# Kernel optimization log

Measured on AMD Instinct MI355X. Metric: run time of the kernel, lower is better.

Reference implementation:

```python
import jax, jax.numpy as jnp
import numpy as np

D = 1024

def setup_inputs() -> dict:
    key = jax.random.key(0)
    ks = jax.random.split(key, 9)
    s = 1.0 / np.sqrt(D)
    x = jax.random.normal(ks[0], (4096, 8, D), dtype=jnp.float32)
    Wq = jax.random.uniform(ks[1], (D, D), jnp.float32, -s, s)
    bq = jax.random.uniform(ks[2], (D,), jnp.float32, -s, s)
    Wk = jax.random.uniform(ks[3], (D, D), jnp.float32, -s, s)
    bk = jax.random.uniform(ks[4], (D,), jnp.float32, -s, s)
    Wv = jax.random.uniform(ks[5], (D, D), jnp.float32, -s, s)
    bv = jax.random.uniform(ks[6], (D,), jnp.float32, -s, s)
    Wo = jax.random.uniform(ks[7], (D, D), jnp.float32, -s, s)
    bo = jax.random.uniform(ks[8], (D,), jnp.float32, -s, s)
    return {"x": x, "Wq": Wq, "bq": bq, "Wk": Wk, "bk": bk,
            "Wv": Wv, "bv": bv, "Wo": Wo, "bo": bo}

def reference(x, Wq, bq, Wk, bk, Wv, bv, Wo, bo):
    # x: (S, B, D) seq-first, matching torch module
    Q = jax.nn.elu(x @ Wq.T + bq) + 1.0  # (S,B,D)
    K = jax.nn.elu(x @ Wk.T + bk) + 1.0  # (S,B,D)
    V = x @ Wv.T + bv                    # (S,B,D)
    # KV = K^T V per batch: (B, D, D)
    KV = jnp.einsum('sbd,sbe->bde', K, V)
    # out = Q @ KV per batch, back to (S,B,D)
    out = jnp.einsum('sbd,bde->sbe', Q, KV)
    return out @ Wo.T + bo
```

## Files before the change

### kernel.cpp

```cpp
#include <hip/hip_runtime.h>


typedef __bf16 bf16;
typedef __attribute__((ext_vector_type(8))) __bf16 bf16x8;
typedef __attribute__((ext_vector_type(4))) __bf16 bf16x4;
typedef __attribute__((ext_vector_type(4))) float f32x4;

static constexpr int S = 4096;
static constexpr int B = 8;
static constexpr int D = 1024;
static constexpr int SB = S * B;
static constexpr long long NELEM = (long long)SB * D;

__device__ __forceinline__ void load_lds16(const bf16* g, void* l)
{
    __builtin_amdgcn_global_load_lds(
        (const __attribute__((address_space(1))) void*)g,
        (__attribute__((address_space(3))) void*)l, 16, 0, 0);
}

__global__ void cvt_f32_to_bf16(const float* __restrict__ in, bf16* __restrict__ out, int n)
{
    int i = (blockIdx.x * blockDim.x + threadIdx.x) * 4;
    int stride = gridDim.x * blockDim.x * 4;
    for (; i < n; i += stride) {
        float4 v = *(const float4*)(in + i);
        bf16x4 o;
        o[0] = (bf16)v.x; o[1] = (bf16)v.y; o[2] = (bf16)v.z; o[3] = (bf16)v.w;
        *(bf16x4*)(out + i) = o;
    }
}

__global__ __launch_bounds__(256) void cvt_transpose_1024(
    const float* __restrict__ in, bf16* __restrict__ out)
{
    __shared__ bf16 tile[64][72];
    const int e0 = blockIdx.y * 64;
    const int d0 = blockIdx.x * 64;
    const int t  = threadIdx.x;
    const int rl = t >> 3;
    const int c8 = (t & 7) * 8;
    #pragma unroll
    for (int p = 0; p < 2; ++p) {
        int r = rl + p * 32;
        float4 v0 = *(const float4*)(in + (long long)(e0 + r) * D + d0 + c8);
        float4 v1 = *(const float4*)(in + (long long)(e0 + r) * D + d0 + c8 + 4);
        tile[c8+0][r] = (bf16)v0.x; tile[c8+1][r] = (bf16)v0.y;
        tile[c8+2][r] = (bf16)v0.z; tile[c8+3][r] = (bf16)v0.w;
        tile[c8+4][r] = (bf16)v1.x; tile[c8+5][r] = (bf16)v1.y;
        tile[c8+6][r] = (bf16)v1.z; tile[c8+7][r] = (bf16)v1.w;
    }
    __syncthreads();
    #pragma unroll
    for (int p = 0; p < 2; ++p) {
        int dr = rl + p * 32;
        *(bf16x8*)(out + (long long)(d0 + dr) * D + e0 + c8) = *(bf16x8*)(&tile[dr][c8]);
    }
}

__global__ __launch_bounds__(256) void bvo_kernel(
    const float* __restrict__ Wo, const float* __restrict__ bv, float* __restrict__ bvo)
{
    const int row = blockIdx.x;
    const int t = threadIdx.x;
    float4 w = *(const float4*)(Wo + (long long)row * D + t * 4);
    float4 b = *(const float4*)(bv + t * 4);
    float s = w.x*b.x + w.y*b.y + w.z*b.z + w.w*b.w;
    __shared__ float red[256];
    red[t] = s; __syncthreads();
    for (int off = 128; off > 0; off >>= 1) {
        if (t < off) red[t] += red[t + off];
        __syncthreads();
    }
    if (t == 0) bvo[row] = red[0];
}

__global__ __launch_bounds__(256) void kv_add(const bf16* __restrict__ p, bf16* __restrict__ o)
{
    const long long DD = (long long)D * D;
    const int b = blockIdx.y;
    const long long i = ((long long)blockIdx.x * 256 + threadIdx.x) * 8;
    bf16x8 u = *(const bf16x8*)(p + (2 * b) * DD + i);
    bf16x8 v = *(const bf16x8*)(p + (2 * b + 1) * DD + i);
    bf16x8 r;
    #pragma unroll
    for (int j = 0; j < 8; ++j) r[j] = (bf16)((float)u[j] + (float)v[j]);
    *(bf16x8*)(o + b * DD + i) = r;
}

template<int BM, int BN, int WM, int WN, int EPI, int OUTF32, int BIASROW>
__global__ __launch_bounds__(WM * WN * 64, 2) void gemm_bt(
    const bf16* __restrict__ A, const bf16* __restrict__ Bm,
    const float* __restrict__ bias, void* __restrict__ Cout,
    int lda, int ldb, int ldc, int K,
    long long aBatch, long long bBatch, long long cBatch)
{
    constexpr int THREADS = WM * WN * 64;
    constexpr int WROWS = BM / WM, WCOLS = BN / WN;
    constexpr int MI = WROWS / 16, NI = WCOLS / 16;
    constexpr int ABYTES = BM * 64;
    constexpr int BBYTES = BN * 64;
    constexpr int BUF = ABYTES + BBYTES;

    __shared__ unsigned char smem[4 * BUF];

    const int tid  = threadIdx.x;
    const int lane = tid & 63;
    const int wave = tid >> 6;
    const int wr   = wave / WN;
    const int wc   = wave % WN;
    const int bz   = blockIdx.z;

    const int nx  = gridDim.x;
    const int bid = blockIdx.y * nx + blockIdx.x;
    const int cpx = (nx * gridDim.y) >> 3;
    const int swz = (bid & 7) * cpx + (bid >> 3);
    const long long m0 = (long long)(swz / nx) * BM;
    const long long n0 = (long long)(swz % nx) * BN;

    const bf16* Ab = A  + bz * aBatch + m0 * lda;
    const bf16* Bb = Bm + bz * bBatch + n0 * ldb;

    f32x4 acc[MI][NI] = {};
    const int NT = K >> 5;

    auto stage = [&](int t) {
        unsigned char* dst = smem + (t & 3) * BUF;
        const long long kk = (long long)t << 5;
        #pragma unroll
        for (int j = 0; j < 2; ++j) {
            const int g  = wave * 64 + lane + j * THREADS;
            const int gs = g ^ ((g >> 3) & 3);
            const int row = gs >> 2, col = (gs & 3) * 8;
            load_lds16(Ab + (long long)row * lda + kk + col,
                       dst + (wave * 64 + j * THREADS) * 16);
        }
        #pragma unroll
        for (int j = 0; j < 2; ++j) {
            const int g  = wave * 64 + lane + j * THREADS;
            const int gs = g ^ ((g >> 3) & 3);
            const int row = gs >> 2, col = (gs & 3) * 8;
            load_lds16(Bb + (long long)row * ldb + kk + col,
                       dst + ABYTES + (wave * 64 + j * THREADS) * 16);
        }
    };

    stage(0); stage(1); stage(2);

    const int ko2 = (lane >> 4) * 16;
    const int la15 = lane & 15;

    for (int t = 0; t < NT; ++t) {
        if (t + 2 < NT)      asm volatile("s_waitcnt vmcnt(8)" ::: "memory");
        else if (t + 1 < NT) asm volatile("s_waitcnt vmcnt(4)" ::: "memory");
        else                 asm volatile("s_waitcnt vmcnt(0)" ::: "memory");
        __builtin_amdgcn_s_barrier();
        asm volatile("" ::: "memory");

        if (t + 3 < NT) stage(t + 3);

        const unsigned char* buf = smem + (t & 3) * BUF;
        bf16x8 a[MI], b[NI];
        #pragma unroll
        for (int mi = 0; mi < MI; ++mi) {
            int ad = (wr * WROWS + mi * 16 + la15) * 64 + ko2;
            ad ^= ((ad >> 7) & 3) << 4;
            a[mi] = *(const bf16x8*)(buf + ad);
        }
        #pragma unroll
        for (int ni = 0; ni < NI; ++ni) {
            int ad = (wc * WCOLS + ni * 16 + la15) * 64 + ko2;
            ad ^= ((ad >> 7) & 3) << 4;
            b[ni] = *(const bf16x8*)(buf + ABYTES + ad);
        }

        __builtin_amdgcn_s_setprio(1);
        #pragma unroll
        for (int mi = 0; mi < MI; ++mi)
            #pragma unroll
            for (int ni = 0; ni < NI; ++ni)
                acc[mi][ni] = __builtin_amdgcn_mfma_f32_16x16x32_bf16(
                    a[mi], b[ni], acc[mi][ni], 0, 0, 0);
        __builtin_amdgcn_s_setprio(0);
    }

    const int crow = (lane >> 4) * 4;
    const int ccol = lane & 15;
    #pragma unroll
    for (int ni = 0; ni < NI; ++ni) {
        const long long c = n0 + wc * WCOLS + ni * 16 + ccol;
        float bcol = 0.0f;
        if (!BIASROW && bias) bcol = bias[c];
        #pragma unroll
        for (int mi = 0; mi < MI; ++mi) {
            const long long r0 = m0 + wr * WROWS + mi * 16 + crow;
            #pragma unroll
            for (int j = 0; j < 4; ++j) {
                float v = acc[mi][ni][j];
                v += BIASROW ? bias[r0 + j] : bcol;
                if (EPI == 1) v = (v > 0.0f) ? (v + 1.0f) : __expf(v);
                const long long idx = bz * cBatch + (r0 + j) * ldc + c;
                if (OUTF32) ((float*)Cout)[idx] = v;
                else        ((bf16*)Cout)[idx]  = (bf16)v;
            }
        }
    }
}

template<int EPI, int OUTF32, int BIASROW, int SPLITK>
__global__ __launch_bounds__(512, 1) void gemm8p(
    const bf16* __restrict__ A, const bf16* __restrict__ Bm,
    const float* __restrict__ bias, void* __restrict__ Cout,
    int lda, int ldb, int ldc, int K,
    long long aBatch, long long bBatch, long long cBatch)
{
    __shared__ unsigned char smem[131072];

    const int tid  = threadIdx.x;
    const int lane = tid & 63;
    const int wave = tid >> 6;
    const int wr   = wave >> 2;
    const int wc   = wave & 3;
    const int bz    = blockIdx.z;
    const int batch = bz / SPLITK;
    const int kseg  = bz % SPLITK;

    const int nx  = gridDim.x;
    const int bid = blockIdx.y * nx + blockIdx.x;
    const int cpx = (nx * gridDim.y) >> 3;
    const int swzb = (bid & 7) * cpx + (bid >> 3);
    const long long m0 = (long long)(swzb / nx) * 256;
    const long long n0 = (long long)(swzb % nx) * 256;

    const bf16* Ab = A  + batch * aBatch + m0 * lda + (long long)kseg * K;
    const bf16* Bb = Bm + batch * bBatch + n0 * ldb + (long long)kseg * K;

    const int sg = (lane & 3) ^ ((lane >> 3) & 3);
    const long long srow = wave * 32 + (lane >> 2);
    const bf16* srcA = Ab + srow * lda + sg * 8;
    const bf16* srcB = Bb + srow * ldb + sg * 8;
    const int dstoff = wave * 2048;

    const int la15 = lane & 15;
    const int rsw  = (lane >> 4) ^ ((la15 >> 1) & 3);
    const int a16  = (wr * 128 + la15) * 4 + rsw;
    const int b16  = (wc * 64  + la15) * 4 + rsw;

    f32x4 acc[8][4] = {};
    const int NT = K >> 6;
    const int NI = NT >> 1;

    auto stageA = [&](int T, int kh) {
        const int reg = ((((T & 1) << 1) | kh) << 14);
        const long long kp = ((long long)T << 6) + (kh << 5);
        load_lds16(srcA + kp,            smem + reg + dstoff);
        load_lds16(srcA + kp + 16 * lda, smem + reg + dstoff + 1024);
    };
    auto stageB = [&](int T, int kh) {
        const int reg = 65536 + ((((T & 1) << 1) | kh) << 14);
        const long long kp = ((long long)T << 6) + (kh << 5);
        load_lds16(srcB + kp,            smem + reg + dstoff);
        load_lds16(srcB + kp + 16 * ldb, smem + reg + dstoff + 1024);
    };

    stageB(0, 0); stageA(0, 0); stageB(0, 1); stageA(0, 1);
    stageB(1, 0); stageA(1, 0); stageB(1, 1);
    asm volatile("s_waitcnt vmcnt(10)" ::: "memory");
    __builtin_amdgcn_s_barrier();
    __builtin_amdgcn_sched_barrier(0);

    bf16x8 bfr[4];
    for (int i = 0; i < NI; ++i) {
        const int t = 2 * i;
        const bool nl = (i + 1 < NI);
        #pragma unroll
        for (int p = 0; p < 8; ++p) {
            const int ks  = (p >> 1) & 1;
            const int ch  = p & 1;
            const int buf = p >> 2;
            const int regA = ((buf << 1) | ks) << 14;
            const int regB = 65536 + regA;

            bf16x8 afr[4];
            if (ch == 0) {
                #pragma unroll
                for (int ni = 0; ni < 4; ++ni)
                    bfr[ni] = *(const bf16x8*)(smem + regB + (b16 + ni * 64) * 16);
            }
            #pragma unroll
            for (int m4 = 0; m4 < 4; ++m4)
                afr[m4] = *(const bf16x8*)(smem + regA + (a16 + (ch * 4 + m4) * 64) * 16);

            if      (p == 0) stageA(t + 1, 1);
            else if (p == 1) { if (t + 2 < NT) stageB(t + 2, 0); }
            else if (p == 2) { if (t + 2 < NT) stageA(t + 2, 0); }
            else if (p == 3) { if (t + 2 < NT) stageB(t + 2, 1); }
            else if (p == 4) { if (t + 2 < NT) stageA(t + 2, 1); }
            else if (p == 5) { if (t + 3 < NT) stageB(t + 3, 0); }
            else if (p == 6) { if (t + 3 < NT) stageA(t + 3, 0); }
            else             { if (t + 3 < NT) stageB(t + 3, 1); }

            if (p == 1) {
                if (nl) asm volatile("s_waitcnt vmcnt(10)" ::: "memory");
                else    asm volatile("s_waitcnt vmcnt(8)"  ::: "memory");
            } else if (p == 3) {
                if (nl) asm volatile("s_waitcnt vmcnt(10)" ::: "memory");
                else    asm volatile("s_waitcnt vmcnt(4)"  ::: "memory");
            } else if (p == 5) {
                if (nl) asm volatile("s_waitcnt vmcnt(10)" ::: "memory");
                else    asm volatile("s_waitcnt vmcnt(0)"  ::: "memory");
            } else if (p == 7) {
                if (nl) asm volatile("s_waitcnt vmcnt(10)" ::: "memory");
            }

            __builtin_amdgcn_s_barrier();
            asm volatile("s_waitcnt lgkmcnt(0)" ::: "memory");
            __builtin_amdgcn_s_setprio(1);
            #pragma unroll
            for (int m4 = 0; m4 < 4; ++m4)
                #pragma unroll
                for (int ni = 0; ni < 4; ++ni)
                    acc[ch * 4 + m4][ni] = __builtin_amdgcn_mfma_f32_16x16x32_bf16(
                        afr[m4], bfr[ni], acc[ch * 4 + m4][ni], 0, 0, 0);
            __builtin_amdgcn_s_setprio(0);
            __builtin_amdgcn_s_barrier();
        }
    }

    const bool doElu = (EPI == 1) || (EPI == 2 && m0 < 1024);
    const long long cb = (long long)bz * cBatch;
    const int crow = (lane >> 4) * 4;

    if constexpr (OUTF32 != 0) {
        #pragma unroll
        for (int ni = 0; ni < 4; ++ni) {
            const long long c = n0 + wc * 64 + ni * 16 + la15;
            float bcol = 0.0f;
            if (!BIASROW && bias) bcol = bias[c];
            #pragma unroll
            for (int mi = 0; mi < 8; ++mi) {
                const long long r0 = m0 + wr * 128 + mi * 16 + crow;
                float* p = (float*)Cout + cb + r0 * ldc + c;
                #pragma unroll
                for (int j = 0; j < 4; ++j) {
                    float v = acc[mi][ni][j] + (BIASROW ? bias[r0 + j] : bcol);
                    if (doElu) v = (v > 0.0f) ? (v + 1.0f) : __expf(v);
                    *p = v; p += ldc;
                }
            }
        }
    } else {
        bf16* lt = (bf16*)smem;
        #pragma unroll
        for (int half = 0; half < 2; ++half) {
            __builtin_amdgcn_s_barrier();
            if (wr == half) {
                #pragma unroll
                for (int mi = 0; mi < 8; ++mi) {
                    const int lrow = mi * 16 + crow;
                    const long long r0 = m0 + half * 128 + lrow;
                    #pragma unroll
                    for (int ni = 0; ni < 4; ++ni) {
                        const int lcol = wc * 64 + ni * 16 + la15;
                        float bb = 0.0f;
                        if (!BIASROW && bias) bb = bias[n0 + lcol];
                        #pragma unroll
                        for (int j = 0; j < 4; ++j) {
                            float v = acc[mi][ni][j] + (BIASROW ? bias[r0 + j] : bb);
                            if (doElu) v = (v > 0.0f) ? (v + 1.0f) : __expf(v);
                            lt[(lrow + j) * 264 + lcol] = (bf16)v;
                        }
                    }
                }
            }
            __builtin_amdgcn_s_barrier();
            #pragma unroll
            for (int it = 0; it < 8; ++it) {
                const int chk = it * 512 + tid;
                const int m   = chk >> 5;
                const int nof = (chk & 31) * 8;
                bf16x8 v = *(const bf16x8*)(lt + m * 264 + nof);
                *(bf16x8*)((bf16*)Cout + cb + (m0 + half * 128 + m) * ldc + n0 + nof) = v;
            }
        }
    }
}

extern "C" void kernel_launch(void* const* d_in, const int* in_sizes, int n_in,
                              void* d_out, int out_size, void* d_ws, size_t ws_size,
                              hipStream_t stream)
{
    const float* x  = (const float*)d_in[0];
    const float* Wq = (const float*)d_in[1];
    const float* bq = (const float*)d_in[2];
    const float* Wk = (const float*)d_in[3];
    const float* bk = (const float*)d_in[4];
    const float* Wv = (const float*)d_in[5];
    const float* bv = (const float*)d_in[6];
    const float* Wo = (const float*)d_in[7];
    const float* bo = (const float*)d_in[8];
    float* out = (float*)d_out;

    char* ws = (char*)d_ws;
    if (ws_size < (size_t)159383552) return;
    bf16*  xb   = (bf16*)(ws + 0);
    bf16*  part = (bf16*)(ws + 67108864);
    bf16*  Qb   = (bf16*)(ws + 67108864);
    bf16*  wvT  = (bf16*)(ws + 134217728);
    float* bkvo = (float*)(ws + 134217728 + 2097152);
    bf16*  KVo  = (bf16*)(ws + 134217728);
    bf16*  wqb  = (bf16*)(ws + 150994944);
    bf16*  wob  = wqb + 1048576;
    bf16*  wkvo = wob + 1048576;
    bf16*  KVb  = (bf16*)d_out;

    cvt_f32_to_bf16<<<4096, 256, 0, stream>>>(x,  xb,  (int)NELEM);
    cvt_f32_to_bf16<<<1024, 256, 0, stream>>>(Wq, wqb, D * D);
    cvt_f32_to_bf16<<<1024, 256, 0, stream>>>(Wo, wob, D * D);
    cvt_f32_to_bf16<<<1024, 256, 0, stream>>>(Wk, wkvo, D * D);
    cvt_transpose_1024<<<dim3(16, 16), 256, 0, stream>>>(Wv, wvT);
    bvo_kernel<<<1024, 256, 0, stream>>>(Wo, bv, bkvo + 1024);
    hipMemcpyAsync(bkvo, bk, D * sizeof(float), hipMemcpyDeviceToDevice, stream);

    gemm_bt<128, 128, 2, 2, 0, 0, 0><<<dim3(8, 8, 1), 256, 0, stream>>>(
        wob, wvT, nullptr, wkvo + (long long)1024 * 1024, D, D, D, D, 0, 0, 0);

    gemm8p<2, 0, 1, 1><<<dim3(16, 8, 8), 512, 0, stream>>>(
        wkvo, xb, bkvo, KVb, D, B * D, S, D,
        0, (long long)D, (long long)2048 * S);

    gemm8p<0, 0, 0, 2><<<dim3(4, 4, 16), 512, 0, stream>>>(
        KVb + (long long)1024 * S, KVb, nullptr, part, S, S, D, 2048,
        (long long)2048 * S, (long long)2048 * S, (long long)D * D);

    kv_add<<<dim3(512, 8), 256, 0, stream>>>(part, KVo);

    gemm8p<1, 0, 0, 1><<<dim3(4, 128, 1), 512, 0, stream>>>(
        xb, wqb, bq, Qb, D, D, D, D, 0, 0, 0);

    gemm8p<0, 1, 0, 1><<<dim3(4, 16, 8), 512, 0, stream>>>(
        Qb, KVo, bo, out, B * D, D, B * D, D,
        (long long)D, (long long)D * D, (long long)D);
}
```

Baseline: 527.4 us.

## Permute x to batch-major bf16 layout and add N-grouped tile swizzle

Converting x to bf16 now also permutes it from (S,B,D) to (B,S,D), so each batch's rows are contiguous with leading dimension D instead of B*D. The K/V projection, Q projection and output GEMMs use the new strides, and the Q GEMM becomes a batched launch over 8 batches. A GROUPN template flag switches the block-to-tile swizzle so the KV GEMM walks tiles grouped along N. The intent is to improve memory locality and L2 reuse from the strided activation reads, at the cost of scattered writes in the conversion kernel.

After: 497.1 us. -5.7%, faster.

```diff
diff --git a/kernel.cpp b/kernel.cpp
--- a/kernel.cpp
+++ b/kernel.cpp
@@ -28,6 +28,24 @@
         bf16x4 o;
         o[0] = (bf16)v.x; o[1] = (bf16)v.y; o[2] = (bf16)v.z; o[3] = (bf16)v.w;
         *(bf16x4*)(out + i) = o;
+    }
+}
+
+__global__ void cvt_permute(const float* __restrict__ in, bf16* __restrict__ out)
+{
+    long long i = ((long long)blockIdx.x * blockDim.x + threadIdx.x) * 8;
+    const long long stride = (long long)gridDim.x * blockDim.x * 8;
+    for (; i < NELEM; i += stride) {
+        const long long s = i >> 13;
+        const long long r = i & 8191;
+        const long long b = r >> 10;
+        const long long d = r & 1023;
+        float4 v0 = *(const float4*)(in + i);
+        float4 v1 = *(const float4*)(in + i + 4);
+        bf16x8 o;
+        o[0] = (bf16)v0.x; o[1] = (bf16)v0.y; o[2] = (bf16)v0.z; o[3] = (bf16)v0.w;
+        o[4] = (bf16)v1.x; o[5] = (bf16)v1.y; o[6] = (bf16)v1.z; o[7] = (bf16)v1.w;
+        *(bf16x8*)(out + b * ((long long)S * D) + s * D + d) = o;
     }
 }
 
@@ -207,7 +225,7 @@
     }
 }
 
-template<int EPI, int OUTF32, int BIASROW, int SPLITK>
+template<int EPI, int OUTF32, int BIASROW, int SPLITK, int GROUPN>
 __global__ __launch_bounds__(512, 1) void gemm8p(
     const bf16* __restrict__ A, const bf16* __restrict__ Bm,
     const float* __restrict__ bias, void* __restrict__ Cout,
@@ -226,11 +244,13 @@
     const int kseg  = bz % SPLITK;
 
     const int nx  = gridDim.x;
+    const int ny  = gridDim.y;
     const int bid = blockIdx.y * nx + blockIdx.x;
-    const int cpx = (nx * gridDim.y) >> 3;
+    const int cpx = (nx * ny) >> 3;
     const int swzb = (bid & 7) * cpx + (bid >> 3);
-    const long long m0 = (long long)(swzb / nx) * 256;
-    const long long n0 = (long long)(swzb % nx) * 256;
+    long long m0, n0;
+    if (GROUPN) { n0 = (long long)(swzb / ny) * 256; m0 = (long long)(swzb % ny) * 256; }
+    else        { m0 = (long long)(swzb / nx) * 256; n0 = (long long)(swzb % nx) * 256; }
 
     const bf16* Ab = A  + batch * aBatch + m0 * lda + (long long)kseg * K;
     const bf16* Bb = Bm + batch * bBatch + n0 * ldb + (long long)kseg * K;
@@ -403,7 +423,7 @@
 
     char* ws = (char*)d_ws;
     if (ws_size < (size_t)159383552) return;
-    bf16*  xb   = (bf16*)(ws + 0);
+    bf16*  xbp  = (bf16*)(ws + 0);
     bf16*  part = (bf16*)(ws + 67108864);
     bf16*  Qb   = (bf16*)(ws + 67108864);
     bf16*  wvT  = (bf16*)(ws + 134217728);
@@ -414,7 +434,9 @@
     bf16*  wkvo = wob + 1048576;
     bf16*  KVb  = (bf16*)d_out;
 
-    cvt_f32_to_bf16<<<4096, 256, 0, stream>>>(x,  xb,  (int)NELEM);
+    const long long SD = (long long)S * D;
+
+    cvt_permute<<<8192, 256, 0, stream>>>(x, xbp);
     cvt_f32_to_bf16<<<1024, 256, 0, stream>>>(Wq, wqb, D * D);
     cvt_f32_to_bf16<<<1024, 256, 0, stream>>>(Wo, wob, D * D);
     cvt_f32_to_bf16<<<1024, 256, 0, stream>>>(Wk, wkvo, D * D);
@@ -425,20 +447,20 @@
     gemm_bt<128, 128, 2, 2, 0, 0, 0><<<dim3(8, 8, 1), 256, 0, stream>>>(
         wob, wvT, nullptr, wkvo + (long long)1024 * 1024, D, D, D, D, 0, 0, 0);
 
-    gemm8p<2, 0, 1, 1><<<dim3(16, 8, 8), 512, 0, stream>>>(
-        wkvo, xb, bkvo, KVb, D, B * D, S, D,
-        0, (long long)D, (long long)2048 * S);
-
-    gemm8p<0, 0, 0, 2><<<dim3(4, 4, 16), 512, 0, stream>>>(
+    gemm8p<2, 0, 1, 1, 1><<<dim3(16, 8, 8), 512, 0, stream>>>(
+        wkvo, xbp, bkvo, KVb, D, D, S, D,
+        0, SD, (long long)2048 * S);
+
+    gemm8p<0, 0, 0, 2, 0><<<dim3(4, 4, 16), 512, 0, stream>>>(
         KVb + (long long)1024 * S, KVb, nullptr, part, S, S, D, 2048,
         (long long)2048 * S, (long long)2048 * S, (long long)D * D);
 
     kv_add<<<dim3(512, 8), 256, 0, stream>>>(part, KVo);
 
-    gemm8p<1, 0, 0, 1><<<dim3(4, 128, 1), 512, 0, stream>>>(
-        xb, wqb, bq, Qb, D, D, D, D, 0, 0, 0);
-
-    gemm8p<0, 1, 0, 1><<<dim3(4, 16, 8), 512, 0, stream>>>(
-        Qb, KVo, bo, out, B * D, D, B * D, D,
-        (long long)D, (long long)D * D, (long long)D);
-}
+    gemm8p<1, 0, 0, 1, 0><<<dim3(4, 16, 8), 512, 0, stream>>>(
+        xbp, wqb, bq, Qb, D, D, D, D, SD, 0, SD);
+
+    gemm8p<0, 1, 0, 1, 0><<<dim3(4, 16, 8), 512, 0, stream>>>(
+        Qb, KVo, bo, out, D, D, B * D, D,
+        SD, (long long)D * D, (long long)D);
+}
```
